# Optimization experiments

Hardware: AMD Instinct MI355X
Metric: run time of the kernel (lower is better)

Reference implementation:

```python
import jax, jax.numpy as jnp
import numpy as np

IMAGE_SIZE = (128, 128)
NUM_SLICES = 4
SLICE_SPACING = 0.1
BACKGROUND = 0.0
CHUNK = 1024
N_GAUSS = 4096
EPS = 1e-6


def setup_inputs() -> dict:
    key = jax.random.key(0)
    k1, k2, k3, k4, k5 = jax.random.split(key, 5)
    return {
        "means": jax.random.uniform(k1, (N_GAUSS, 3), dtype=jnp.float32),
        "scales": jax.random.uniform(k2, (N_GAUSS, 3), dtype=jnp.float32),
        "rotations": jax.random.normal(k3, (N_GAUSS, 4), dtype=jnp.float32),
        "opacities": jax.random.uniform(k4, (N_GAUSS, 1), dtype=jnp.float32),
        "features": jax.random.uniform(k5, (N_GAUSS, 1), dtype=jnp.float32),
    }


def _quat_to_rot(q):
    # q: [N,4] (w,x,y,z) -> [N,3,3]
    q = q / jnp.linalg.norm(q, axis=1, keepdims=True)
    w, x, y, z = q[:, 0], q[:, 1], q[:, 2], q[:, 3]
    r0 = jnp.stack([1 - 2 * (y * y + z * z), 2 * (x * y - w * z), 2 * (x * z + w * y)], axis=-1)
    r1 = jnp.stack([2 * (x * y + w * z), 1 - 2 * (x * x + z * z), 2 * (y * z - w * x)], axis=-1)
    r2 = jnp.stack([2 * (x * z - w * y), 2 * (y * z + w * x), 1 - 2 * (x * x + y * y)], axis=-1)
    return jnp.stack([r0, r1, r2], axis=-2)


def _forward(means, scales, rotations, opacities, features):
    H, W = IMAGE_SIZE
    dtype = means.dtype
    P = H * W

    # 3D covariance: Sigma = (R S)(R S)^T
    R = _quat_to_rot(rotations)
    RS = R * scales[:, None, :]
    cov = RS @ jnp.swapaxes(RS, 1, 2)  # [N,3,3]

    # slice z positions and shared pixel grid
    total_depth = (NUM_SLICES - 1) * SLICE_SPACING
    zs = jnp.linspace(-total_depth / 2, total_depth / 2, NUM_SLICES)
    yy, xx = jnp.meshgrid(jnp.linspace(-1, 1, H), jnp.linspace(-1, 1, W), indexing="ij")
    grid = jnp.stack([xx, yy], axis=-1).reshape(P, 2).astype(dtype)

    # conditional (marginal-at-z) 2D covariance, slice independent
    sxy = cov[:, :2, :2]                     # [N,2,2]
    sxz = cov[:, :2, 2]                      # [N,2]
    szz = cov[:, 2, 2]                       # [N]
    sigma2d = sxy - (sxz[:, :, None] * sxz[:, None, :]) / (szz + EPS)[:, None, None]
    sigma2d = sigma2d + EPS * jnp.eye(2, dtype=dtype)
    a, b = sigma2d[:, 0, 0], sigma2d[:, 0, 1]
    c, d = sigma2d[:, 1, 0], sigma2d[:, 1, 1]
    det = a * d - b * c
    inv2d = jnp.stack([jnp.stack([d, -b], -1), jnp.stack([-c, a], -1)], -2) / det[:, None, None]

    max_dist = 3.0 * scales[:, 2].max()

    nch = N_GAUSS // CHUNK
    rs = lambda t: t.reshape((nch, CHUNK) + t.shape[1:])
    chunks = (rs(means), rs(inv2d), rs(sxz), rs(szz), rs(opacities[:, 0]), rs(features[:, 0]))

    def render_slice(slice_z):
        def body(carry, ch):
            img, acc = carry
            mu, invk, sxzk, szzk, op, ft = ch
            mask = (jnp.abs(mu[:, 2] - slice_z) < max_dist).astype(dtype)  # all-pass by construction
            zoff = slice_z - mu[:, 2]
            mu2d = mu[:, :2] + sxzk / (szzk + EPS)[:, None] * zoff[:, None]  # [K,2]
            off = grid[:, None, :] - mu2d[None, :, :]                        # [P,K,2]
            maha = jnp.einsum("pki,kij,pkj->pk", off, invk, off)
            g = jnp.exp(-0.5 * maha) * mask[None, :]                         # [P,K]
            weight = (1 - acc)[:, None] * (g * op[None, :])
            img = img + (weight * (g * ft[None, :])).sum(-1)
            acc = acc + weight.sum(-1)
            return (img, acc), None

        init = (jnp.zeros(P, dtype), jnp.zeros(P, dtype))
        (img, acc), _ = jax.lax.scan(body, init, chunks)
        img = img + (1 - acc) * BACKGROUND
        return img.reshape(H, W)

    return jnp.stack([render_slice(zs[s]) for s in range(NUM_SLICES)], axis=0)


def reference(means, scales, rotations, opacities, features):
    return _forward(means, scales, rotations, opacities, features)
```

## Files before the change

### kernel.cpp

```cpp
#include <hip/hip_runtime.h>


#define EPSV 1e-6f
#define NG   4096
#define PP   16384
#define NSL  4
#define SPLIT 16
#define GPC  64

typedef float v2f __attribute__((ext_vector_type(2)));

static __device__ __forceinline__ v2f splat(float s) { v2f r; r.x = s; r.y = s; return r; }

__global__ void prep_kernel(const float* __restrict__ means,
                            const float* __restrict__ scales,
                            const float* __restrict__ rots,
                            const float* __restrict__ ops,
                            const float* __restrict__ fts,
                            float4* __restrict__ gdata) {
    __shared__ float red[256];
    int tid = threadIdx.x;

    float m = -1e30f;
    for (int i = tid; i < NG; i += 256) m = fmaxf(m, scales[i*3+2]);
    red[tid] = m;
    __syncthreads();
    for (int s = 128; s > 0; s >>= 1) {
        if (tid < s) red[tid] = fmaxf(red[tid], red[tid+s]);
        __syncthreads();
    }
    float maxd = 3.0f * red[0];

    int g = blockIdx.x * 256 + tid;
    if (g >= NG) return;

    float qw = rots[g*4+0], qx = rots[g*4+1], qy = rots[g*4+2], qz = rots[g*4+3];
    float inorm = rsqrtf(qw*qw + qx*qx + qy*qy + qz*qz);
    qw *= inorm; qx *= inorm; qy *= inorm; qz *= inorm;

    float s0 = scales[g*3+0], s1 = scales[g*3+1], s2 = scales[g*3+2];

    float r00 = 1.f - 2.f*(qy*qy + qz*qz), r01 = 2.f*(qx*qy - qw*qz), r02 = 2.f*(qx*qz + qw*qy);
    float r10 = 2.f*(qx*qy + qw*qz), r11 = 1.f - 2.f*(qx*qx + qz*qz), r12 = 2.f*(qy*qz - qw*qx);
    float r20 = 2.f*(qx*qz - qw*qy), r21 = 2.f*(qy*qz + qw*qx), r22 = 1.f - 2.f*(qx*qx + qy*qy);

    float a00 = r00*s0, a01 = r01*s1, a02 = r02*s2;
    float a10 = r10*s0, a11 = r11*s1, a12 = r12*s2;
    float a20 = r20*s0, a21 = r21*s1, a22 = r22*s2;

    float c00 = a00*a00 + a01*a01 + a02*a02;
    float c01 = a00*a10 + a01*a11 + a02*a12;
    float c02 = a00*a20 + a01*a21 + a02*a22;
    float c11 = a10*a10 + a11*a11 + a12*a12;
    float c12 = a10*a20 + a11*a21 + a12*a22;
    float c22 = a20*a20 + a21*a21 + a22*a22;

    float izz = 1.0f / (c22 + EPSV);
    float kx = c02 * izz, ky = c12 * izz;
    float sa = c00 - c02*c02*izz + EPSV;
    float sb = c01 - c02*c12*izz;
    float sd = c11 - c12*c12*izz + EPSV;
    float det = sa*sd - sb*sb;
    float idet = 1.0f / det;

    const float C0 = -0.72134752044448170f;
    float qa = C0 * sd * idet;
    float qb = C0 * (-2.0f * sb * idet);
    float qd = C0 * sa * idet;

    float mx = means[g*3+0], my = means[g*3+1], mz = means[g*3+2];
    float op = ops[g], ft = fts[g];

    #pragma unroll
    for (int s = 0; s < NSL; ++s) {
        float z = -0.15f + 0.1f * (float)s;
        float zoff = z - mz;
        float m2x = mx + kx * zoff;
        float m2y = my + ky * zoff;
        bool live = (fabsf(mz - z) < maxd) && (op > 1e-12f);
        float lop  = live ? __log2f(op) : -__builtin_inff();
        float ftop = live ? ft / op     : 0.f;
        float4* o = gdata + ((size_t)(s*NG + g)) * 2;
        o[0] = make_float4(-m2x, -m2y, qa, qb);
        o[1] = make_float4( qd,   lop,  ftop, 0.f);
    }
}

__global__ __launch_bounds__(1024, 4)
void render_kernel(const float4* __restrict__ gdata, float* __restrict__ out) {
    __shared__ float parts[SPLIT][64][9];

    int tid   = threadIdx.x;
    int lane  = tid & 63;
    int split = __builtin_amdgcn_readfirstlane(tid >> 6);
    int slice = blockIdx.x >> 6;
    int r0    = (blockIdx.x & 63) * 2;

    const float DL = 2.0f / 127.0f;
    v2f xP;  xP.x = -1.0f + (float)lane * DL;  xP.y = xP.x + 64.0f * DL;
    v2f yP0 = splat(-1.0f + (float)r0 * DL);
    v2f yP1 = splat(-1.0f + (float)(r0 + 1) * DL);

    const float4* gs = gdata + (size_t)slice * NG * 2;

    float img = 0.f, acc = 0.f;

    #pragma unroll
    for (int c = 0; c < 4; ++c) {
        const float4* p = gs + (size_t)(c * 1024 + split * GPC) * 2;
        v2f a10 = {0.f,0.f}, a11 = {0.f,0.f}, a20 = {0.f,0.f}, a21 = {0.f,0.f};
        #pragma unroll 8
        for (int g = 0; g < GPC; ++g) {
            float4 A = p[2*g+0];
            float4 B = p[2*g+1];
            v2f dx  = xP  + splat(A.x);
            v2f dy0 = yP0 + splat(A.y);
            v2f dy1 = yP1 + splat(A.y);
            v2f t0  = __builtin_elementwise_fma(splat(A.z), dx, splat(A.w) * dy0);
            v2f t1  = __builtin_elementwise_fma(splat(A.z), dx, splat(A.w) * dy1);
            v2f e0  = __builtin_elementwise_fma(splat(B.x) * dy0, dy0, splat(B.y));
            v2f e1  = __builtin_elementwise_fma(splat(B.x) * dy1, dy1, splat(B.y));
            v2f mm0 = __builtin_elementwise_fma(dx, t0, e0);
            v2f mm1 = __builtin_elementwise_fma(dx, t1, e1);
            v2f gv0, gv1;
            gv0.x = __builtin_amdgcn_exp2f(mm0.x);
            gv0.y = __builtin_amdgcn_exp2f(mm0.y);
            gv1.x = __builtin_amdgcn_exp2f(mm1.x);
            gv1.y = __builtin_amdgcn_exp2f(mm1.y);
            a10 += gv0;
            a11 += gv1;
            a20 = __builtin_elementwise_fma(gv0 * gv0, splat(B.z), a20);
            a21 = __builtin_elementwise_fma(gv1 * gv1, splat(B.z), a21);
        }
        __syncthreads();
        parts[split][lane][0] = a10.x;
        parts[split][lane][1] = a10.y;
        parts[split][lane][2] = a11.x;
        parts[split][lane][3] = a11.y;
        parts[split][lane][4] = a20.x;
        parts[split][lane][5] = a20.y;
        parts[split][lane][6] = a21.x;
        parts[split][lane][7] = a21.y;
        __syncthreads();
        if (split < 4) {
            float S1 = 0.f, S2 = 0.f;
            #pragma unroll
            for (int s = 0; s < SPLIT; ++s) {
                S1 += parts[s][lane][split];
                S2 += parts[s][lane][4 + split];
            }
            float om = 1.0f - acc;
            img = fmaf(om, S2, img);
            acc = fmaf(om, S1, acc);
        }
    }

    if (split < 4)
        out[slice * PP + (r0 + (split >> 1)) * 128 + (split & 1) * 64 + lane] = img;
}

extern "C" void kernel_launch(void* const* d_in, const int* in_sizes, int n_in,
                              void* d_out, int out_size, void* d_ws, size_t ws_size,
                              hipStream_t stream) {
    const float* means  = (const float*)d_in[0];
    const float* scales = (const float*)d_in[1];
    const float* rots   = (const float*)d_in[2];
    const float* ops    = (const float*)d_in[3];
    const float* fts    = (const float*)d_in[4];
    float* out = (float*)d_out;

    float4* gdata = (float4*)d_ws;

    prep_kernel<<<NG/256, 256, 0, stream>>>(means, scales, rots, ops, fts, gdata);
    render_kernel<<<NSL*64, 1024, 0, stream>>>(gdata, out);
}
```

Before: 130.7 us.

## Defer split reduction to one final barrier and reorder gaussian layout per split

The render kernel now stores every chunk's partial sums in a larger shared-memory array. It runs a single barrier and the front-to-back compositing reduction once at the end, instead of two barriers per chunk. The prep kernel permutes gaussian storage so each split's 256 gaussians are contiguous, and the inner loop moves from packed 2-wide vector math to scalar FMAs. The much larger LDS footprint (about 135 KB per block) and the relaxed launch bounds may cut occupancy. Dropping packed FP32 ops may also increase instruction count.

Result: no change. 131.2 us (+0.4%).

```diff
diff --git a/kernel.cpp b/kernel.cpp
--- a/kernel.cpp
+++ b/kernel.cpp
@@ -7,10 +7,7 @@
 #define NSL  4
 #define SPLIT 16
 #define GPC  64
-
-typedef float v2f __attribute__((ext_vector_type(2)));
-
-static __device__ __forceinline__ v2f splat(float s) { v2f r; r.x = s; r.y = s; return r; }
+#define GPS  256
 
 __global__ void prep_kernel(const float* __restrict__ means,
                             const float* __restrict__ scales,
@@ -71,6 +68,12 @@
     float mx = means[g*3+0], my = means[g*3+1], mz = means[g*3+2];
     float op = ops[g], ft = fts[g];
 
+    int chunk = g >> 10;
+    int w     = g & 1023;
+    int split = w >> 6;
+    int idx   = w & 63;
+    int pos   = split * GPS + chunk * GPC + idx;
+
     #pragma unroll
     for (int s = 0; s < NSL; ++s) {
         float z = -0.15f + 0.1f * (float)s;
@@ -80,15 +83,15 @@
         bool live = (fabsf(mz - z) < maxd) && (op > 1e-12f);
         float lop  = live ? __log2f(op) : -__builtin_inff();
         float ftop = live ? ft / op     : 0.f;
-        float4* o = gdata + ((size_t)(s*NG + g)) * 2;
+        float4* o = gdata + ((size_t)(s*NG + pos)) * 2;
         o[0] = make_float4(-m2x, -m2y, qa, qb);
         o[1] = make_float4( qd,   lop,  ftop, 0.f);
     }
 }
 
-__global__ __launch_bounds__(1024, 4)
+__global__ __launch_bounds__(1024, 1)
 void render_kernel(const float4* __restrict__ gdata, float* __restrict__ out) {
-    __shared__ float parts[SPLIT][64][9];
+    __shared__ float parts[SPLIT][64][33];
 
     int tid   = threadIdx.x;
     int lane  = tid & 63;
@@ -97,66 +100,67 @@
     int r0    = (blockIdx.x & 63) * 2;
 
     const float DL = 2.0f / 127.0f;
-    v2f xP;  xP.x = -1.0f + (float)lane * DL;  xP.y = xP.x + 64.0f * DL;
-    v2f yP0 = splat(-1.0f + (float)r0 * DL);
-    v2f yP1 = splat(-1.0f + (float)(r0 + 1) * DL);
+    float x0 = -1.0f + (float)lane * DL;
+    float x1 = x0 + 64.0f * DL;
+    float y0 = -1.0f + (float)r0 * DL;
+    float y1 = y0 + DL;
 
-    const float4* gs = gdata + (size_t)slice * NG * 2;
-
-    float img = 0.f, acc = 0.f;
+    const float4* p = gdata + ((size_t)slice * NG + split * GPS) * 2;
 
     #pragma unroll
     for (int c = 0; c < 4; ++c) {
-        const float4* p = gs + (size_t)(c * 1024 + split * GPC) * 2;
-        v2f a10 = {0.f,0.f}, a11 = {0.f,0.f}, a20 = {0.f,0.f}, a21 = {0.f,0.f};
+        float s100 = 0.f, s101 = 0.f, s110 = 0.f, s111 = 0.f;
+        float s200 = 0.f, s201 = 0.f, s210 = 0.f, s211 = 0.f;
         #pragma unroll 8
         for (int g = 0; g < GPC; ++g) {
-            float4 A = p[2*g+0];
-            float4 B = p[2*g+1];
-            v2f dx  = xP  + splat(A.x);
-            v2f dy0 = yP0 + splat(A.y);
-            v2f dy1 = yP1 + splat(A.y);
-            v2f t0  = __builtin_elementwise_fma(splat(A.z), dx, splat(A.w) * dy0);
-            v2f t1  = __builtin_elementwise_fma(splat(A.z), dx, splat(A.w) * dy1);
-            v2f e0  = __builtin_elementwise_fma(splat(B.x) * dy0, dy0, splat(B.y));
-            v2f e1  = __builtin_elementwise_fma(splat(B.x) * dy1, dy1, splat(B.y));
-            v2f mm0 = __builtin_elementwise_fma(dx, t0, e0);
-            v2f mm1 = __builtin_elementwise_fma(dx, t1, e1);
-            v2f gv0, gv1;
-            gv0.x = __builtin_amdgcn_exp2f(mm0.x);
-            gv0.y = __builtin_amdgcn_exp2f(mm0.y);
-            gv1.x = __builtin_amdgcn_exp2f(mm1.x);
-            gv1.y = __builtin_amdgcn_exp2f(mm1.y);
-            a10 += gv0;
-            a11 += gv1;
-            a20 = __builtin_elementwise_fma(gv0 * gv0, splat(B.z), a20);
-            a21 = __builtin_elementwise_fma(gv1 * gv1, splat(B.z), a21);
+            float4 A = p[(c*GPC + g)*2 + 0];
+            float4 B = p[(c*GPC + g)*2 + 1];
+            float dy0 = y0 + A.y;
+            float dy1 = y1 + A.y;
+            float Qb0 = A.w * dy0;
+            float Qb1 = A.w * dy1;
+            float R0  = fmaf(B.x * dy0, dy0, B.y);
+            float R1  = fmaf(B.x * dy1, dy1, B.y);
+            float dx0 = x0 + A.x;
+            float dx1 = x1 + A.x;
+            float m00 = fmaf(fmaf(A.z, dx0, Qb0), dx0, R0);
+            float m01 = fmaf(fmaf(A.z, dx1, Qb1), dx1, R1);
+            float m10 = fmaf(fmaf(A.z, dx0, Qb1), dx0, R1);
+            float m11 = fmaf(fmaf(A.z, dx1, Qb1), dx1, R1);
+            m01 = fmaf(fmaf(A.z, dx1, Qb0), dx1, R0);
+            float g00 = __builtin_amdgcn_exp2f(m00);
+            float g01 = __builtin_amdgcn_exp2f(m01);
+            float g10 = __builtin_amdgcn_exp2f(m10);
+            float g11 = __builtin_amdgcn_exp2f(m11);
+            s100 += g00;  s101 += g01;  s110 += g10;  s111 += g11;
+            s200 = fmaf(g00*g00, B.z, s200);
+            s201 = fmaf(g01*g01, B.z, s201);
+            s210 = fmaf(g10*g10, B.z, s210);
+            s211 = fmaf(g11*g11, B.z, s211);
         }
-        __syncthreads();
-        parts[split][lane][0] = a10.x;
-        parts[split][lane][1] = a10.y;
-        parts[split][lane][2] = a11.x;
-        parts[split][lane][3] = a11.y;
-        parts[split][lane][4] = a20.x;
-        parts[split][lane][5] = a20.y;
-        parts[split][lane][6] = a21.x;
-        parts[split][lane][7] = a21.y;
-        __syncthreads();
-        if (split < 4) {
+        float* q = &parts[split][lane][c*8];
+        q[0] = s100;  q[1] = s101;  q[2] = s110;  q[3] = s111;
+        q[4] = s200;  q[5] = s201;  q[6] = s210;  q[7] = s211;
+    }
+
+    __syncthreads();
+
+    if (split < 4) {
+        float img = 0.f, acc = 0.f;
+        #pragma unroll
+        for (int c = 0; c < 4; ++c) {
             float S1 = 0.f, S2 = 0.f;
             #pragma unroll
             for (int s = 0; s < SPLIT; ++s) {
-                S1 += parts[s][lane][split];
-                S2 += parts[s][lane][4 + split];
+                S1 += parts[s][lane][c*8 + split];
+                S2 += parts[s][lane][c*8 + 4 + split];
             }
             float om = 1.0f - acc;
             img = fmaf(om, S2, img);
             acc = fmaf(om, S1, acc);
         }
+        out[slice * PP + (r0 + (split >> 1)) * 128 + (split & 1) * 64 + lane] = img;
     }
-
-    if (split < 4)
-        out[slice * PP + (r0 + (split >> 1)) * 128 + (split & 1) * 64 + lane] = img;
 }
 
 extern "C" void kernel_launch(void* const* d_in, const int* in_sizes, int n_in,
```

## Split Gaussian work across blocks and combine partials in a separate kernel

Applied to the files above, without the earlier changes.

The render kernel no longer has each block reduce partial sums through shared memory with barriers per chunk. Each block now handles 32 rows for one chunk-segment of 128 Gaussians and writes per-pixel partial (sum, weighted sum) pairs to workspace. A new combine kernel applies the chunk-wise transmittance recurrence over 32 segments per pixel. This removes the shared-memory barriers and idle waves, and gives more blocks and higher occupancy, at the cost of an extra kernel launch and about 16 MB of partial traffic through global memory.

Measured after the change: 128.7 us. About the same (-1.6%).

```diff
diff --git a/kernel.cpp b/kernel.cpp
--- a/kernel.cpp
+++ b/kernel.cpp
@@ -5,8 +5,8 @@
 #define NG   4096
 #define PP   16384
 #define NSL  4
-#define SPLIT 16
-#define GPC  64
+#define SEGS 8
+#define GSEG 128
 
 typedef float v2f __attribute__((ext_vector_type(2)));
 
@@ -86,77 +86,76 @@
     }
 }
 
-__global__ __launch_bounds__(1024, 4)
-void render_kernel(const float4* __restrict__ gdata, float* __restrict__ out) {
-    __shared__ float parts[SPLIT][64][9];
-
+__global__ __launch_bounds__(1024, 8)
+void render_kernel(const float4* __restrict__ gdata, float2* __restrict__ part) {
     int tid   = threadIdx.x;
     int lane  = tid & 63;
-    int split = __builtin_amdgcn_readfirstlane(tid >> 6);
-    int slice = blockIdx.x >> 6;
-    int r0    = (blockIdx.x & 63) * 2;
+    int w     = __builtin_amdgcn_readfirstlane(tid >> 6);
+    int b     = blockIdx.x;
+    int pxg   = b >> 5;
+    int split = b & 31;
+    int slice = pxg >> 2;
+    int r0    = (pxg & 3) * 32 + w * 2;
+    int chunk = split >> 3;
+    int seg   = split & 7;
 
     const float DL = 2.0f / 127.0f;
     v2f xP;  xP.x = -1.0f + (float)lane * DL;  xP.y = xP.x + 64.0f * DL;
     v2f yP0 = splat(-1.0f + (float)r0 * DL);
     v2f yP1 = splat(-1.0f + (float)(r0 + 1) * DL);
 
-    const float4* gs = gdata + (size_t)slice * NG * 2;
+    const float4* p = gdata + ((size_t)slice * NG + chunk * 1024 + seg * GSEG) * 2;
 
+    v2f a10 = {0.f,0.f}, a11 = {0.f,0.f}, a20 = {0.f,0.f}, a21 = {0.f,0.f};
+    #pragma unroll 8
+    for (int g = 0; g < GSEG; ++g) {
+        float4 A = p[2*g+0];
+        float4 B = p[2*g+1];
+        v2f dx  = xP  + splat(A.x);
+        v2f dy0 = yP0 + splat(A.y);
+        v2f dy1 = yP1 + splat(A.y);
+        v2f t0  = __builtin_elementwise_fma(splat(A.z), dx, splat(A.w) * dy0);
+        v2f t1  = __builtin_elementwise_fma(splat(A.z), dx, splat(A.w) * dy1);
+        v2f e0  = __builtin_elementwise_fma(splat(B.x) * dy0, dy0, splat(B.y));
+        v2f e1  = __builtin_elementwise_fma(splat(B.x) * dy1, dy1, splat(B.y));
+        v2f mm0 = __builtin_elementwise_fma(dx, t0, e0);
+        v2f mm1 = __builtin_elementwise_fma(dx, t1, e1);
+        v2f gv0, gv1;
+        gv0.x = __builtin_amdgcn_exp2f(mm0.x);
+        gv0.y = __builtin_amdgcn_exp2f(mm0.y);
+        gv1.x = __builtin_amdgcn_exp2f(mm1.x);
+        gv1.y = __builtin_amdgcn_exp2f(mm1.y);
+        a10 += gv0;
+        a11 += gv1;
+        a20 = __builtin_elementwise_fma(gv0 * gv0, splat(B.z), a20);
+        a21 = __builtin_elementwise_fma(gv1 * gv1, splat(B.z), a21);
+    }
+
+    size_t o = ((size_t)(slice * PP + r0 * 128 + lane)) * 32 + chunk * 8 + seg;
+    part[o           ] = make_float2(a10.x, a20.x);
+    part[o +  64 * 32] = make_float2(a10.y, a20.y);
+    part[o + 128 * 32] = make_float2(a11.x, a21.x);
+    part[o + 192 * 32] = make_float2(a11.y, a21.y);
+}
+
+__global__ __launch_bounds__(256)
+void combine_kernel(const float2* __restrict__ part, float* __restrict__ out) {
+    int px = blockIdx.x * 256 + threadIdx.x;
+    const float2* q = part + (size_t)px * 32;
     float img = 0.f, acc = 0.f;
-
     #pragma unroll
     for (int c = 0; c < 4; ++c) {
-        const float4* p = gs + (size_t)(c * 1024 + split * GPC) * 2;
-        v2f a10 = {0.f,0.f}, a11 = {0.f,0.f}, a20 = {0.f,0.f}, a21 = {0.f,0.f};
-        #pragma unroll 8
-        for (int g = 0; g < GPC; ++g) {
-            float4 A = p[2*g+0];
-            float4 B = p[2*g+1];
-            v2f dx  = xP  + splat(A.x);
-            v2f dy0 = yP0 + splat(A.y);
-            v2f dy1 = yP1 + splat(A.y);
-            v2f t0  = __builtin_elementwise_fma(splat(A.z), dx, splat(A.w) * dy0);
-            v2f t1  = __builtin_elementwise_fma(splat(A.z), dx, splat(A.w) * dy1);
-            v2f e0  = __builtin_elementwise_fma(splat(B.x) * dy0, dy0, splat(B.y));
-            v2f e1  = __builtin_elementwise_fma(splat(B.x) * dy1, dy1, splat(B.y));
-            v2f mm0 = __builtin_elementwise_fma(dx, t0, e0);
-            v2f mm1 = __builtin_elementwise_fma(dx, t1, e1);
-            v2f gv0, gv1;
-            gv0.x = __builtin_amdgcn_exp2f(mm0.x);
-            gv0.y = __builtin_amdgcn_exp2f(mm0.y);
-            gv1.x = __builtin_amdgcn_exp2f(mm1.x);
-            gv1.y = __builtin_amdgcn_exp2f(mm1.y);
-            a10 += gv0;
-            a11 += gv1;
-            a20 = __builtin_elementwise_fma(gv0 * gv0, splat(B.z), a20);
-            a21 = __builtin_elementwise_fma(gv1 * gv1, splat(B.z), a21);
+        float S1 = 0.f, S2 = 0.f;
+        #pragma unroll
+        for (int s = 0; s < SEGS; ++s) {
+            float2 v = q[c*8 + s];
+            S1 += v.x;  S2 += v.y;
         }
-        __syncthreads();
-        parts[split][lane][0] = a10.x;
-        parts[split][lane][1] = a10.y;
-        parts[split][lane][2] = a11.x;
-        parts[split][lane][3] = a11.y;
-        parts[split][lane][4] = a20.x;
-        parts[split][lane][5] = a20.y;
-        parts[split][lane][6] = a21.x;
-        parts[split][lane][7] = a21.y;
-        __syncthreads();
-        if (split < 4) {
-            float S1 = 0.f, S2 = 0.f;
-            #pragma unroll
-            for (int s = 0; s < SPLIT; ++s) {
-                S1 += parts[s][lane][split];
-                S2 += parts[s][lane][4 + split];
-            }
-            float om = 1.0f - acc;
-            img = fmaf(om, S2, img);
-            acc = fmaf(om, S1, acc);
-        }
+        float om = 1.0f - acc;
+        img = fmaf(om, S2, img);
+        acc = fmaf(om, S1, acc);
     }
-
-    if (split < 4)
-        out[slice * PP + (r0 + (split >> 1)) * 128 + (split & 1) * 64 + lane] = img;
+    out[px] = img;
 }
 
 extern "C" void kernel_launch(void* const* d_in, const int* in_sizes, int n_in,
@@ -170,7 +169,9 @@
     float* out = (float*)d_out;
 
     float4* gdata = (float4*)d_ws;
+    float2* part  = (float2*)((char*)d_ws + (size_t)NSL*NG*32);
 
     prep_kernel<<<NG/256, 256, 0, stream>>>(means, scales, rots, ops, fts, gdata);
-    render_kernel<<<NSL*64, 1024, 0, stream>>>(gdata, out);
+    render_kernel<<<512, 1024, 0, stream>>>(gdata, part);
+    combine_kernel<<<NSL*PP/256, 256, 0, stream>>>(part, out);
 }
```
